# Kernel tuning notes

Hardware: AMD Instinct MI355X
Metric: run time of the kernel (lower is better)

## Reference

```python
import jax, jax.numpy as jnp
import numpy as np

B, Nv, Ne, Dv, De, Du = 8, 4096, 32768, 128, 128, 128
Dep, Dvp, Dup = 128, 128, 128


def setup_inputs() -> dict:
    key = jax.random.key(0)
    ks = jax.random.split(key, 11)
    s = 0.02
    return {
        "nodes": jax.random.normal(ks[0], (B, Nv, Dv), jnp.float32),
        "edges": jax.random.normal(ks[1], (B, Ne, De), jnp.float32),
        "global_u": jax.random.normal(ks[2], (B, Du), jnp.float32),
        "edge_rs": jax.random.randint(ks[3], (B, Ne, 2), 0, Nv, jnp.int32),
        "edge_masks": jax.random.randint(ks[4], (B, Ne, 1), 0, 2, jnp.int32),
        "W_edge": jax.random.normal(ks[5], (De + 2 * Dv + Du, Dep), jnp.float32) * s,
        "b_edge": jnp.zeros((Dep,), jnp.float32),
        "W_node": jax.random.normal(ks[6], (Dep + Dv + Du, Dvp), jnp.float32) * s,
        "b_node": jnp.zeros((Dvp,), jnp.float32),
        "W_glob": jax.random.normal(ks[7], (Dep + Dvp + Du, Dup), jnp.float32) * s,
        "b_glob": jnp.zeros((Dup,), jnp.float32),
    }


def reference(nodes, edges, global_u, edge_rs, edge_masks,
              W_edge, b_edge, W_node, b_node, W_glob, b_glob):
    recv = edge_rs[..., 0]  # (B,Ne)
    send = edge_rs[..., 1]
    # gather receiver / sender node features: (B,Ne,Dv)
    r_nodes = jnp.take_along_axis(nodes, jnp.broadcast_to(recv[..., None], (B, Ne, Dv)), axis=1)
    s_nodes = jnp.take_along_axis(nodes, jnp.broadcast_to(send[..., None], (B, Ne, Dv)), axis=1)
    u_e = jnp.broadcast_to(global_u[:, None, :], (B, Ne, Du))

    # edge block: MLP on concat -> (B,Ne,Dep)
    edge_in = jnp.concatenate([edges, r_nodes, s_nodes, u_e], -1)
    edges_p = jax.nn.relu(edge_in @ W_edge + b_edge)

    # e2v merge: masked segment-sum of edges onto receiver nodes -> (B,Nv,Dep)
    mask = edge_masks.astype(edges_p.dtype)  # (B,Ne,1)
    e2v = jax.vmap(lambda e, r: jax.ops.segment_sum(e, r, num_segments=Nv))(edges_p * mask, recv)

    # node block
    u_n = jnp.broadcast_to(global_u[:, None, :], (B, Nv, Du))
    node_in = jnp.concatenate([e2v, nodes, u_n], -1)
    nodes_p = jax.nn.relu(node_in @ W_node + b_node)

    # global block: sum-pool edges and nodes
    e2u = edges_p.sum(axis=1)  # (B,Dep)
    v2u = nodes_p.sum(axis=1)  # (B,Dvp)
    global_in = jnp.concatenate([e2u, v2u, global_u], -1)
    global_u_p = jax.nn.relu(global_in @ W_glob + b_glob)

    return (nodes_p, edges_p, global_u_p)
```

## Files before the change

kernel.cpp:

```cpp
#include <hip/hip_runtime.h>
#include <hip/hip_bf16.h>

#define B  8
#define NV 4096
#define NE 32768
#define D  128
#define KE2 384
#define KN2 256
#define KG 384

using short8 = __attribute__((ext_vector_type(8))) short;
using f32x4  = __attribute__((ext_vector_type(4))) float;

__device__ inline unsigned short f2bf(float f) {
    unsigned u = __builtin_bit_cast(unsigned, f);
    u += 0x7FFFu + ((u >> 16) & 1u);
    return (unsigned short)(u >> 16);
}

__device__ inline short8 cvt8(float4 a, float4 b) {
    union { __hip_bfloat162 h[4]; short8 v; } u;
    u.h[0] = __float22bfloat162_rn(make_float2(a.x, a.y));
    u.h[1] = __float22bfloat162_rn(make_float2(a.z, a.w));
    u.h[2] = __float22bfloat162_rn(make_float2(b.x, b.y));
    u.h[3] = __float22bfloat162_rn(make_float2(b.z, b.w));
    return u.v;
}

__global__ __launch_bounds__(256) void prep_weights(
    const float* __restrict__ We, const float* __restrict__ Wn,
    unsigned short* __restrict__ WtE, unsigned short* __restrict__ WtN)
{
    const int idx = blockIdx.x * 256 + threadIdx.x;
    {
        const int n = idx / KE2, k = idx % KE2;
        WtE[idx] = f2bf(We[(size_t)k * D + n]);
    }
    if (idx < 128 * KN2) {
        const int n = idx >> 8, k = idx & 255;
        WtN[idx] = f2bf(Wn[(size_t)k * D + n]);
    }
}

__global__ __launch_bounds__(128) void bias_kernel(
    const float* __restrict__ gu,
    const float* __restrict__ We, const float* __restrict__ be,
    const float* __restrict__ Wn, const float* __restrict__ bn,
    float* __restrict__ bias_e, float* __restrict__ bias_n)
{
    const int b = blockIdx.x, n = threadIdx.x;
    float se = be[n], sn = bn[n];
    for (int k = 0; k < D; ++k) {
        const float uk = gu[(size_t)b * D + k];
        se += uk * We[(size_t)(KE2 + k) * D + n];
        sn += uk * Wn[(size_t)(KN2 + k) * D + n];
    }
    bias_e[(size_t)b * D + n] = se;
    bias_n[(size_t)b * D + n] = sn;
}

__global__ __launch_bounds__(256) void hist_kernel(
    const int* __restrict__ edge_rs, const int* __restrict__ edge_masks,
    int* __restrict__ cnt)
{
    const int idx = blockIdx.x * 256 + threadIdx.x;
    if (edge_masks[idx]) {
        const int b = idx >> 15;
        const int r = edge_rs[2 * idx];
        atomicAdd(cnt + b * NV + r, 1);
    }
}

__global__ __launch_bounds__(1024) void scan_kernel(
    const int* __restrict__ cnt, int* __restrict__ off, int* __restrict__ cur)
{
    const int b = blockIdx.x, t = threadIdx.x;
    __shared__ int part[1024];
    int4 c = *(const int4*)(cnt + b * NV + t * 4);
    const int s0 = c.x, s1 = s0 + c.y, s2 = s1 + c.z, s3 = s2 + c.w;
    part[t] = s3;
    __syncthreads();
    #pragma unroll
    for (int d = 1; d < 1024; d <<= 1) {
        const int v = (t >= d) ? part[t - d] : 0;
        __syncthreads();
        part[t] += v;
        __syncthreads();
    }
    const int base = part[t] - s3;
    int* o = off + b * (NV + 1) + t * 4;
    o[0] = base; o[1] = base + s0; o[2] = base + s1; o[3] = base + s2;
    int4 cc = { base, base + s0, base + s1, base + s2 };
    *(int4*)(cur + b * NV + t * 4) = cc;
    if (t == 1023) off[b * (NV + 1) + NV] = part[1023];
}

__global__ __launch_bounds__(256) void scatter_kernel(
    const int* __restrict__ edge_rs, const int* __restrict__ edge_masks,
    int* __restrict__ cur, int* __restrict__ elist)
{
    const int idx = blockIdx.x * 256 + threadIdx.x;
    if (edge_masks[idx]) {
        const int b = idx >> 15;
        const int e = idx & (NE - 1);
        const int r = edge_rs[2 * idx];
        const int pos = atomicAdd(cur + b * NV + r, 1);
        elist[b * NE + pos] = e;
    }
}

__global__ __launch_bounds__(512, 4) void edge_kernel(
    const float* __restrict__ nodes,
    const float* __restrict__ edges,
    const int*   __restrict__ edge_rs,
    const unsigned short* __restrict__ WtE,
    const float* __restrict__ bias_e,
    float* __restrict__ edges_p,
    float* __restrict__ pe)
{
    __shared__ unsigned short Albuf[2][128 * 64];
    __shared__ unsigned short Wlbuf[2][128 * 64];

    const int tid = threadIdx.x;
    const int b   = blockIdx.y;
    const int e0  = blockIdx.x * 128;

    const int srow = tid >> 2;
    const int sq   = tid & 3;
    const int sX   = (srow & 7) << 3;

    const int2 rs = ((const int2*)edge_rs)[(size_t)b * NE + e0 + srow];
    const float* aseg0 = edges + ((size_t)b * NE + e0 + srow) * D;
    const float* aseg1 = nodes + ((size_t)b * NV + rs.x) * D;
    const float* aseg2 = nodes + ((size_t)b * NV + rs.y) * D;

    const int lane = tid & 63;
    const int wv   = tid >> 6;
    const int wr   = wv >> 2, wc = wv & 3;
    const int lc   = lane & 15, lg = lane >> 4;
    const int lX   = (lc & 7) << 3;

    float4 av[2];
    short8 wstg[2];

    auto loadA = [&](int t) {
        const float* seg = (t < 2) ? aseg0 : (t < 4) ? aseg1 : aseg2;
        const float* src = seg + (t & 1) * 64 + sq * 16;
        av[0] = *(const float4*)(src);
        av[1] = *(const float4*)(src + 4);
        av[0] = av[0];
    };
    auto loadA2 = [&](int t, float4& c0, float4& c1) {
        const float* seg = (t < 2) ? aseg0 : (t < 4) ? aseg1 : aseg2;
        const float* src = seg + (t & 1) * 64 + sq * 16;
        c0 = *(const float4*)(src + 8);
        c1 = *(const float4*)(src + 12);
    };
    auto loadW = [&](int t) {
        const unsigned short* src = WtE + (size_t)srow * KE2 + t * 64 + sq * 16;
        wstg[0] = *(const short8*)(src);
        wstg[1] = *(const short8*)(src + 8);
    };

    float4 av2[2];
    auto writeStage = [&](int buf) {
        unsigned short* Al = Albuf[buf];
        unsigned short* Wl = Wlbuf[buf];
        const int g0 = sq * 16;
        *(short8*)(Al + srow * 64 + ((g0    ) ^ sX)) = cvt8(av[0], av[1]);
        *(short8*)(Al + srow * 64 + ((g0 + 8) ^ sX)) = cvt8(av2[0], av2[1]);
        *(short8*)(Wl + srow * 64 + ((g0    ) ^ sX)) = wstg[0];
        *(short8*)(Wl + srow * 64 + ((g0 + 8) ^ sX)) = wstg[1];
    };

    f32x4 acc[4][2] = {};
    auto compute = [&](int buf) {
        const unsigned short* Al = Albuf[buf];
        const unsigned short* Wl = Wlbuf[buf];
        #pragma unroll
        for (int ksub = 0; ksub < 2; ++ksub) {
            const int k = ksub * 32 + lg * 8;
            short8 afr[4], bfr[2];
            #pragma unroll
            for (int mt = 0; mt < 4; ++mt)
                afr[mt] = *(const short8*)(Al + (wr * 64 + mt * 16 + lc) * 64 + (k ^ lX));
            #pragma unroll
            for (int nt = 0; nt < 2; ++nt)
                bfr[nt] = *(const short8*)(Wl + (wc * 32 + nt * 16 + lc) * 64 + (k ^ lX));
            #pragma unroll
            for (int mt = 0; mt < 4; ++mt)
                #pragma unroll
                for (int nt = 0; nt < 2; ++nt)
                    acc[mt][nt] = __builtin_amdgcn_mfma_f32_16x16x32_bf16(
                                      afr[mt], bfr[nt], acc[mt][nt], 0, 0, 0);
        }
    };

    loadA(0); loadA2(0, av2[0], av2[1]); loadW(0); writeStage(0);
    __syncthreads();
    #pragma unroll
    for (int t = 0; t < 6; ++t) {
        if (t < 5) { loadA(t + 1); loadA2(t + 1, av2[0], av2[1]); loadW(t + 1); }
        compute(t & 1);
        if (t < 5) writeStage((t + 1) & 1);
        __syncthreads();
    }

    #pragma unroll
    for (int nt = 0; nt < 2; ++nt) {
        const int col = wc * 32 + nt * 16 + lc;
        const float bias = bias_e[(size_t)b * D + col];
        float csum = 0.f;
        #pragma unroll
        for (int mt = 0; mt < 4; ++mt)
            #pragma unroll
            for (int r = 0; r < 4; ++r) {
                const int row = wr * 64 + mt * 16 + lg * 4 + r;
                const float v = fmaxf(acc[mt][nt][r] + bias, 0.f);
                edges_p[((size_t)b * NE + e0 + row) * D + col] = v;
                csum += v;
            }
        csum += __shfl_xor(csum, 16);
        csum += __shfl_xor(csum, 32);
        if (lg == 0)
            pe[(((size_t)b * 256 + blockIdx.x) * 2 + wr) * D + col] = csum;
    }
}

__global__ __launch_bounds__(512, 4) void node_kernel(
    const float* __restrict__ nodes,
    const float* __restrict__ edges_p,
    const int*   __restrict__ off,
    const int*   __restrict__ elist,
    const unsigned short* __restrict__ WtN,
    const float* __restrict__ bias_n,
    float* __restrict__ nodes_p,
    float* __restrict__ pn)
{
    __shared__ unsigned short Albuf[2][128 * 64];
    __shared__ unsigned short Wlbuf[2][128 * 64];

    const int tid = threadIdx.x;
    const int b   = blockIdx.y;
    const int n0  = blockIdx.x * 128;

    const int srow = tid >> 2;
    const int sq   = tid & 3;
    const int sX   = (srow & 7) << 3;

    const int vtx = n0 + srow;
    const int p0  = off[b * (NV + 1) + vtx];
    const int p1  = off[b * (NV + 1) + vtx + 1];
    const float* nsrc = nodes + ((size_t)b * NV + vtx) * D;

    const int lane = tid & 63;
    const int wv   = tid >> 6;
    const int wr   = wv >> 2, wc = wv & 3;
    const int lc   = lane & 15, lg = lane >> 4;
    const int lX   = (lc & 7) << 3;

    float4 av[2], av2[2];
    short8 wstg[2];

    auto loadA = [&](int t) {
        if (t < 2) {
            float4 s0 = {}, s1 = {}, s2 = {}, s3 = {};
            const int koff = (t & 1) * 64 + sq * 16;
            for (int p = p0; p < p1; ++p) {
                const int e = elist[b * NE + p];
                const float* src = edges_p + ((size_t)b * NE + e) * D + koff;
                const float4 x0 = *(const float4*)(src);
                const float4 x1 = *(const float4*)(src + 4);
                const float4 x2 = *(const float4*)(src + 8);
                const float4 x3 = *(const float4*)(src + 12);
                s0.x += x0.x; s0.y += x0.y; s0.z += x0.z; s0.w += x0.w;
                s1.x += x1.x; s1.y += x1.y; s1.z += x1.z; s1.w += x1.w;
                s2.x += x2.x; s2.y += x2.y; s2.z += x2.z; s2.w += x2.w;
                s3.x += x3.x; s3.y += x3.y; s3.z += x3.z; s3.w += x3.w;
            }
            av[0] = s0; av[1] = s1; av2[0] = s2; av2[1] = s3;
        } else {
            const float* src = nsrc + (t - 2) * 64 + sq * 16;
            av[0]  = *(const float4*)(src);
            av[1]  = *(const float4*)(src + 4);
            av2[0] = *(const float4*)(src + 8);
            av2[1] = *(const float4*)(src + 12);
        }
    };
    auto loadW = [&](int t) {
        const unsigned short* src = WtN + (size_t)srow * KN2 + t * 64 + sq * 16;
        wstg[0] = *(const short8*)(src);
        wstg[1] = *(const short8*)(src + 8);
    };
    auto writeStage = [&](int buf) {
        unsigned short* Al = Albuf[buf];
        unsigned short* Wl = Wlbuf[buf];
        const int g0 = sq * 16;
        *(short8*)(Al + srow * 64 + ((g0    ) ^ sX)) = cvt8(av[0], av[1]);
        *(short8*)(Al + srow * 64 + ((g0 + 8) ^ sX)) = cvt8(av2[0], av2[1]);
        *(short8*)(Wl + srow * 64 + ((g0    ) ^ sX)) = wstg[0];
        *(short8*)(Wl + srow * 64 + ((g0 + 8) ^ sX)) = wstg[1];
    };

    f32x4 acc[4][2] = {};
    auto compute = [&](int buf) {
        const unsigned short* Al = Albuf[buf];
        const unsigned short* Wl = Wlbuf[buf];
        #pragma unroll
        for (int ksub = 0; ksub < 2; ++ksub) {
            const int k = ksub * 32 + lg * 8;
            short8 afr[4], bfr[2];
            #pragma unroll
            for (int mt = 0; mt < 4; ++mt)
                afr[mt] = *(const short8*)(Al + (wr * 64 + mt * 16 + lc) * 64 + (k ^ lX));
            #pragma unroll
            for (int nt = 0; nt < 2; ++nt)
                bfr[nt] = *(const short8*)(Wl + (wc * 32 + nt * 16 + lc) * 64 + (k ^ lX));
            #pragma unroll
            for (int mt = 0; mt < 4; ++mt)
                #pragma unroll
                for (int nt = 0; nt < 2; ++nt)
                    acc[mt][nt] = __builtin_amdgcn_mfma_f32_16x16x32_bf16(
                                      afr[mt], bfr[nt], acc[mt][nt], 0, 0, 0);
        }
    };

    loadA(0); loadW(0); writeStage(0);
    __syncthreads();
    #pragma unroll
    for (int t = 0; t < 4; ++t) {
        if (t < 3) { loadA(t + 1); loadW(t + 1); }
        compute(t & 1);
        if (t < 3) writeStage((t + 1) & 1);
        __syncthreads();
    }

    #pragma unroll
    for (int nt = 0; nt < 2; ++nt) {
        const int col = wc * 32 + nt * 16 + lc;
        const float bias = bias_n[(size_t)b * D + col];
        float csum = 0.f;
        #pragma unroll
        for (int mt = 0; mt < 4; ++mt)
            #pragma unroll
            for (int r = 0; r < 4; ++r) {
                const int row = wr * 64 + mt * 16 + lg * 4 + r;
                const float v = fmaxf(acc[mt][nt][r] + bias, 0.f);
                nodes_p[((size_t)b * NV + n0 + row) * D + col] = v;
                csum += v;
            }
        csum += __shfl_xor(csum, 16);
        csum += __shfl_xor(csum, 32);
        if (lg == 0)
            pn[(((size_t)b * 32 + blockIdx.x) * 2 + wr) * D + col] = csum;
    }
}

__global__ __launch_bounds__(128) void reduce_kernel(
    const float* __restrict__ pe, const float* __restrict__ pn,
    float* __restrict__ e2u, float* __restrict__ v2u)
{
    const int b = blockIdx.x, j = threadIdx.x;
    float s = 0.f;
    for (int i = 0; i < 512; ++i) s += pe[((size_t)b * 512 + i) * D + j];
    e2u[(size_t)b * D + j] = s;
    float t = 0.f;
    for (int i = 0; i < 64; ++i) t += pn[((size_t)b * 64 + i) * D + j];
    v2u[(size_t)b * D + j] = t;
}

__global__ __launch_bounds__(128) void glob_kernel(
    const float* __restrict__ e2u,
    const float* __restrict__ v2u,
    const float* __restrict__ gu,
    const float* __restrict__ W_glob,
    const float* __restrict__ b_glob,
    float* __restrict__ glob_p)
{
    __shared__ float gin[KG];
    const int b = blockIdx.x;
    const int j = threadIdx.x;

    gin[j      ] = e2u[(size_t)b * D + j];
    gin[j + 128] = v2u[(size_t)b * D + j];
    gin[j + 256] = gu [(size_t)b * D + j];
    __syncthreads();

    float acc = b_glob[j];
    #pragma unroll 4
    for (int k = 0; k < KG; ++k)
        acc += gin[k] * W_glob[(size_t)k * D + j];
    glob_p[(size_t)b * D + j] = fmaxf(acc, 0.f);
}

extern "C" void kernel_launch(void* const* d_in, const int* in_sizes, int n_in,
                              void* d_out, int out_size, void* d_ws, size_t ws_size,
                              hipStream_t stream) {
    const float* nodes      = (const float*)d_in[0];
    const float* edges      = (const float*)d_in[1];
    const float* gu         = (const float*)d_in[2];
    const int*   edge_rs    = (const int*)d_in[3];
    const int*   edge_masks = (const int*)d_in[4];
    const float* W_edge     = (const float*)d_in[5];
    const float* b_edge     = (const float*)d_in[6];
    const float* W_node     = (const float*)d_in[7];
    const float* b_node     = (const float*)d_in[8];
    const float* W_glob     = (const float*)d_in[9];
    const float* b_glob     = (const float*)d_in[10];

    float* out     = (float*)d_out;
    float* nodes_p = out;
    float* edges_p = out + (size_t)B * NV * D;
    float* glob_p  = edges_p + (size_t)B * NE * D;

    int*   cnt    = (int*)d_ws;
    int*   off    = cnt + (size_t)B * NV;
    int*   cur    = off + (size_t)B * (NV + 1);
    int*   elist  = cur + (size_t)B * NV;
    float* e2u    = (float*)(elist + (size_t)B * NE);
    float* v2u    = e2u + (size_t)B * D;
    float* bias_e = v2u + (size_t)B * D;
    float* bias_n = bias_e + (size_t)B * D;
    float* pe     = bias_n + (size_t)B * D;
    float* pn     = pe + (size_t)B * 512 * D;
    unsigned short* WtE = (unsigned short*)(pn + (size_t)B * 64 * D);
    unsigned short* WtN = WtE + 128 * KE2;

    hipMemsetAsync(cnt, 0, (size_t)B * NV * sizeof(int), stream);

    prep_weights<<<(128 * KE2) / 256, 256, 0, stream>>>(W_edge, W_node, WtE, WtN);
    bias_kernel<<<B, 128, 0, stream>>>(gu, W_edge, b_edge, W_node, b_node, bias_e, bias_n);
    hist_kernel<<<(B * NE) / 256, 256, 0, stream>>>(edge_rs, edge_masks, cnt);
    scan_kernel<<<B, 1024, 0, stream>>>(cnt, off, cur);
    scatter_kernel<<<(B * NE) / 256, 256, 0, stream>>>(edge_rs, edge_masks, cur, elist);

    dim3 eg(NE / 128, B);
    edge_kernel<<<eg, 512, 0, stream>>>(nodes, edges, edge_rs,
                                        WtE, bias_e, edges_p, pe);
    dim3 ng(NV / 128, B);
    node_kernel<<<ng, 512, 0, stream>>>(nodes, edges_p, off, elist,
                                        WtN, bias_n, nodes_p, pn);
    reduce_kernel<<<B, 128, 0, stream>>>(pe, pn, e2u, v2u);
    glob_kernel<<<B, 128, 0, stream>>>(e2u, v2u, gu, W_glob, b_glob, glob_p);
}
```

Baseline: 199.4 us.

## Load weight fragments directly from global memory, dropping LDS weight staging

Both the edge and node GEMM kernels stop staging the bf16 weight tiles through shared memory. Each wave now reads its B fragments straight from global memory, which the cache should serve since the weights are small and shared by all blocks. This halves LDS use per block, and the launch bounds are raised to allow more resident blocks per CU. The trade-off is global-load latency inside the MFMA loop that is no longer hidden by the double buffer, plus possibly more register pressure under the tighter occupancy bound.

```diff
diff --git a/kernel.cpp b/kernel.cpp
--- a/kernel.cpp
+++ b/kernel.cpp
@@ -109,7 +109,7 @@
     }
 }
 
-__global__ __launch_bounds__(512, 4) void edge_kernel(
+__global__ __launch_bounds__(512, 8) void edge_kernel(
     const float* __restrict__ nodes,
     const float* __restrict__ edges,
     const int*   __restrict__ edge_rs,
@@ -119,7 +119,6 @@
     float* __restrict__ pe)
 {
     __shared__ unsigned short Albuf[2][128 * 64];
-    __shared__ unsigned short Wlbuf[2][128 * 64];
 
     const int tid = threadIdx.x;
     const int b   = blockIdx.y;
@@ -140,53 +139,37 @@
     const int lc   = lane & 15, lg = lane >> 4;
     const int lX   = (lc & 7) << 3;
 
-    float4 av[2];
-    short8 wstg[2];
+    float4 av[2], av2[2];
 
     auto loadA = [&](int t) {
         const float* seg = (t < 2) ? aseg0 : (t < 4) ? aseg1 : aseg2;
         const float* src = seg + (t & 1) * 64 + sq * 16;
-        av[0] = *(const float4*)(src);
-        av[1] = *(const float4*)(src + 4);
-        av[0] = av[0];
-    };
-    auto loadA2 = [&](int t, float4& c0, float4& c1) {
-        const float* seg = (t < 2) ? aseg0 : (t < 4) ? aseg1 : aseg2;
-        const float* src = seg + (t & 1) * 64 + sq * 16;
-        c0 = *(const float4*)(src + 8);
-        c1 = *(const float4*)(src + 12);
-    };
-    auto loadW = [&](int t) {
-        const unsigned short* src = WtE + (size_t)srow * KE2 + t * 64 + sq * 16;
-        wstg[0] = *(const short8*)(src);
-        wstg[1] = *(const short8*)(src + 8);
-    };
-
-    float4 av2[2];
+        av[0]  = *(const float4*)(src);
+        av[1]  = *(const float4*)(src + 4);
+        av2[0] = *(const float4*)(src + 8);
+        av2[1] = *(const float4*)(src + 12);
+    };
     auto writeStage = [&](int buf) {
         unsigned short* Al = Albuf[buf];
-        unsigned short* Wl = Wlbuf[buf];
         const int g0 = sq * 16;
         *(short8*)(Al + srow * 64 + ((g0    ) ^ sX)) = cvt8(av[0], av[1]);
         *(short8*)(Al + srow * 64 + ((g0 + 8) ^ sX)) = cvt8(av2[0], av2[1]);
-        *(short8*)(Wl + srow * 64 + ((g0    ) ^ sX)) = wstg[0];
-        *(short8*)(Wl + srow * 64 + ((g0 + 8) ^ sX)) = wstg[1];
     };
 
     f32x4 acc[4][2] = {};
-    auto compute = [&](int buf) {
+    auto compute = [&](int buf, int t) {
         const unsigned short* Al = Albuf[buf];
-        const unsigned short* Wl = Wlbuf[buf];
         #pragma unroll
         for (int ksub = 0; ksub < 2; ++ksub) {
             const int k = ksub * 32 + lg * 8;
             short8 afr[4], bfr[2];
             #pragma unroll
+            for (int nt = 0; nt < 2; ++nt)
+                bfr[nt] = *(const short8*)(WtE + (size_t)(wc * 32 + nt * 16 + lc) * KE2
+                                               + t * 64 + k);
+            #pragma unroll
             for (int mt = 0; mt < 4; ++mt)
                 afr[mt] = *(const short8*)(Al + (wr * 64 + mt * 16 + lc) * 64 + (k ^ lX));
-            #pragma unroll
-            for (int nt = 0; nt < 2; ++nt)
-                bfr[nt] = *(const short8*)(Wl + (wc * 32 + nt * 16 + lc) * 64 + (k ^ lX));
             #pragma unroll
             for (int mt = 0; mt < 4; ++mt)
                 #pragma unroll
@@ -196,12 +179,12 @@
         }
     };
 
-    loadA(0); loadA2(0, av2[0], av2[1]); loadW(0); writeStage(0);
+    loadA(0); writeStage(0);
     __syncthreads();
     #pragma unroll
     for (int t = 0; t < 6; ++t) {
-        if (t < 5) { loadA(t + 1); loadA2(t + 1, av2[0], av2[1]); loadW(t + 1); }
-        compute(t & 1);
+        if (t < 5) loadA(t + 1);
+        compute(t & 1, t);
         if (t < 5) writeStage((t + 1) & 1);
         __syncthreads();
     }
@@ -227,7 +210,7 @@
     }
 }
 
-__global__ __launch_bounds__(512, 4) void node_kernel(
+__global__ __launch_bounds__(512, 6) void node_kernel(
     const float* __restrict__ nodes,
     const float* __restrict__ edges_p,
     const int*   __restrict__ off,
@@ -238,7 +221,6 @@
     float* __restrict__ pn)
 {
     __shared__ unsigned short Albuf[2][128 * 64];
-    __shared__ unsigned short Wlbuf[2][128 * 64];
 
     const int tid = threadIdx.x;
     const int b   = blockIdx.y;
@@ -260,7 +242,6 @@
     const int lX   = (lc & 7) << 3;
 
     float4 av[2], av2[2];
-    short8 wstg[2];
 
     auto loadA = [&](int t) {
         if (t < 2) {
@@ -287,35 +268,27 @@
             av2[1] = *(const float4*)(src + 12);
         }
     };
-    auto loadW = [&](int t) {
-        const unsigned short* src = WtN + (size_t)srow * KN2 + t * 64 + sq * 16;
-        wstg[0] = *(const short8*)(src);
-        wstg[1] = *(const short8*)(src + 8);
-    };
     auto writeStage = [&](int buf) {
         unsigned short* Al = Albuf[buf];
-        unsigned short* Wl = Wlbuf[buf];
         const int g0 = sq * 16;
         *(short8*)(Al + srow * 64 + ((g0    ) ^ sX)) = cvt8(av[0], av[1]);
         *(short8*)(Al + srow * 64 + ((g0 + 8) ^ sX)) = cvt8(av2[0], av2[1]);
-        *(short8*)(Wl + srow * 64 + ((g0    ) ^ sX)) = wstg[0];
-        *(short8*)(Wl + srow * 64 + ((g0 + 8) ^ sX)) = wstg[1];
     };
 
     f32x4 acc[4][2] = {};
-    auto compute = [&](int buf) {
+    auto compute = [&](int buf, int t) {
         const unsigned short* Al = Albuf[buf];
-        const unsigned short* Wl = Wlbuf[buf];
         #pragma unroll
         for (int ksub = 0; ksub < 2; ++ksub) {
             const int k = ksub * 32 + lg * 8;
             short8 afr[4], bfr[2];
             #pragma unroll
+            for (int nt = 0; nt < 2; ++nt)
+                bfr[nt] = *(const short8*)(WtN + (size_t)(wc * 32 + nt * 16 + lc) * KN2
+                                               + t * 64 + k);
+            #pragma unroll
             for (int mt = 0; mt < 4; ++mt)
                 afr[mt] = *(const short8*)(Al + (wr * 64 + mt * 16 + lc) * 64 + (k ^ lX));
-            #pragma unroll
-            for (int nt = 0; nt < 2; ++nt)
-                bfr[nt] = *(const short8*)(Wl + (wc * 32 + nt * 16 + lc) * 64 + (k ^ lX));
             #pragma unroll
             for (int mt = 0; mt < 4; ++mt)
                 #pragma unroll
@@ -325,12 +298,12 @@
         }
     };
 
-    loadA(0); loadW(0); writeStage(0);
+    loadA(0); writeStage(0);
     __syncthreads();
     #pragma unroll
     for (int t = 0; t < 4; ++t) {
-        if (t < 3) { loadA(t + 1); loadW(t + 1); }
-        compute(t & 1);
+        if (t < 3) loadA(t + 1);
+        compute(t & 1, t);
         if (t < 3) writeStage((t + 1) & 1);
         __syncthreads();
     }
```

After: 301.3 us. 1.51x slower.

## Shrink edge kernel LDS, retile node kernel to 64 rows, split reduce

Applied to the files above, without the earlier changes.

The edge kernel drops the double-buffered weight tile for a single buffer and adds an extra barrier before each stage write. This cuts LDS use and raises the occupancy hint from 4 to 6 blocks per CU. The node kernel moves to 64-vertex tiles with 256 threads, so the grid has twice as many blocks to spread the irregular segment-sum gather across CUs, and the reduce kernel now uses two halves plus a shared-memory combine. The trade-off is an extra sync per stage in the edge kernel, which serializes the stage write against compute, and more register pressure from the tighter launch bound.

```diff
diff --git a/kernel.cpp b/kernel.cpp
--- a/kernel.cpp
+++ b/kernel.cpp
@@ -109,7 +109,7 @@
     }
 }
 
-__global__ __launch_bounds__(512, 4) void edge_kernel(
+__global__ __launch_bounds__(512, 6) void edge_kernel(
     const float* __restrict__ nodes,
     const float* __restrict__ edges,
     const int*   __restrict__ edge_rs,
@@ -119,7 +119,7 @@
     float* __restrict__ pe)
 {
     __shared__ unsigned short Albuf[2][128 * 64];
-    __shared__ unsigned short Wlbuf[2][128 * 64];
+    __shared__ unsigned short Wlbuf[128 * 64];
 
     const int tid = threadIdx.x;
     const int b   = blockIdx.y;
@@ -140,53 +140,47 @@
     const int lc   = lane & 15, lg = lane >> 4;
     const int lX   = (lc & 7) << 3;
 
-    float4 av[2];
+    float4 av[2], av2[2];
     short8 wstg[2];
 
     auto loadA = [&](int t) {
         const float* seg = (t < 2) ? aseg0 : (t < 4) ? aseg1 : aseg2;
         const float* src = seg + (t & 1) * 64 + sq * 16;
-        av[0] = *(const float4*)(src);
-        av[1] = *(const float4*)(src + 4);
-        av[0] = av[0];
-    };
-    auto loadA2 = [&](int t, float4& c0, float4& c1) {
-        const float* seg = (t < 2) ? aseg0 : (t < 4) ? aseg1 : aseg2;
-        const float* src = seg + (t & 1) * 64 + sq * 16;
-        c0 = *(const float4*)(src + 8);
-        c1 = *(const float4*)(src + 12);
+        av[0]  = *(const float4*)(src);
+        av[1]  = *(const float4*)(src + 4);
+        av2[0] = *(const float4*)(src + 8);
+        av2[1] = *(const float4*)(src + 12);
     };
     auto loadW = [&](int t) {
         const unsigned short* src = WtE + (size_t)srow * KE2 + t * 64 + sq * 16;
         wstg[0] = *(const short8*)(src);
         wstg[1] = *(const short8*)(src + 8);
     };
-
-    float4 av2[2];
-    auto writeStage = [&](int buf) {
+    auto writeStageA = [&](int buf) {
         unsigned short* Al = Albuf[buf];
-        unsigned short* Wl = Wlbuf[buf];
         const int g0 = sq * 16;
         *(short8*)(Al + srow * 64 + ((g0    ) ^ sX)) = cvt8(av[0], av[1]);
         *(short8*)(Al + srow * 64 + ((g0 + 8) ^ sX)) = cvt8(av2[0], av2[1]);
-        *(short8*)(Wl + srow * 64 + ((g0    ) ^ sX)) = wstg[0];
-        *(short8*)(Wl + srow * 64 + ((g0 + 8) ^ sX)) = wstg[1];
+    };
+    auto writeStageW = [&]() {
+        const int g0 = sq * 16;
+        *(short8*)(Wlbuf + srow * 64 + ((g0    ) ^ sX)) = wstg[0];
+        *(short8*)(Wlbuf + srow * 64 + ((g0 + 8) ^ sX)) = wstg[1];
     };
 
     f32x4 acc[4][2] = {};
     auto compute = [&](int buf) {
         const unsigned short* Al = Albuf[buf];
-        const unsigned short* Wl = Wlbuf[buf];
         #pragma unroll
         for (int ksub = 0; ksub < 2; ++ksub) {
             const int k = ksub * 32 + lg * 8;
             short8 afr[4], bfr[2];
             #pragma unroll
+            for (int nt = 0; nt < 2; ++nt)
+                bfr[nt] = *(const short8*)(Wlbuf + (wc * 32 + nt * 16 + lc) * 64 + (k ^ lX));
+            #pragma unroll
             for (int mt = 0; mt < 4; ++mt)
                 afr[mt] = *(const short8*)(Al + (wr * 64 + mt * 16 + lc) * 64 + (k ^ lX));
-            #pragma unroll
-            for (int nt = 0; nt < 2; ++nt)
-                bfr[nt] = *(const short8*)(Wl + (wc * 32 + nt * 16 + lc) * 64 + (k ^ lX));
             #pragma unroll
             for (int mt = 0; mt < 4; ++mt)
                 #pragma unroll
@@ -196,14 +190,18 @@
         }
     };
 
-    loadA(0); loadA2(0, av2[0], av2[1]); loadW(0); writeStage(0);
+    loadA(0); loadW(0); writeStageA(0); writeStageW();
     __syncthreads();
     #pragma unroll
     for (int t = 0; t < 6; ++t) {
-        if (t < 5) { loadA(t + 1); loadA2(t + 1, av2[0], av2[1]); loadW(t + 1); }
+        if (t < 5) { loadA(t + 1); loadW(t + 1); }
         compute(t & 1);
-        if (t < 5) writeStage((t + 1) & 1);
-        __syncthreads();
+        if (t < 5) {
+            __syncthreads();
+            writeStageA((t + 1) & 1);
+            writeStageW();
+            __syncthreads();
+        }
     }
 
     #pragma unroll
@@ -227,7 +225,7 @@
     }
 }
 
-__global__ __launch_bounds__(512, 4) void node_kernel(
+__global__ __launch_bounds__(256, 3) void node_kernel(
     const float* __restrict__ nodes,
     const float* __restrict__ edges_p,
     const int*   __restrict__ off,
@@ -237,35 +235,38 @@
     float* __restrict__ nodes_p,
     float* __restrict__ pn)
 {
-    __shared__ unsigned short Albuf[2][128 * 64];
+    __shared__ unsigned short Albuf[2][64 * 64];
     __shared__ unsigned short Wlbuf[2][128 * 64];
 
     const int tid = threadIdx.x;
     const int b   = blockIdx.y;
-    const int n0  = blockIdx.x * 128;
-
-    const int srow = tid >> 2;
-    const int sq   = tid & 3;
-    const int sX   = (srow & 7) << 3;
-
-    const int vtx = n0 + srow;
+    const int n0  = blockIdx.x * 64;
+
+    const int srowA = tid >> 2;
+    const int sqA   = tid & 3;
+    const int sXA   = (srowA & 7) << 3;
+    const int srowW = tid >> 1;
+    const int sqW   = tid & 1;
+    const int sXW   = (srowW & 7) << 3;
+
+    const int vtx = n0 + srowA;
     const int p0  = off[b * (NV + 1) + vtx];
     const int p1  = off[b * (NV + 1) + vtx + 1];
     const float* nsrc = nodes + ((size_t)b * NV + vtx) * D;
 
     const int lane = tid & 63;
     const int wv   = tid >> 6;
-    const int wr   = wv >> 2, wc = wv & 3;
+    const int wr   = wv >> 1, wc = wv & 1;
     const int lc   = lane & 15, lg = lane >> 4;
     const int lX   = (lc & 7) << 3;
 
     float4 av[2], av2[2];
-    short8 wstg[2];
+    short8 wstg[4];
 
     auto loadA = [&](int t) {
         if (t < 2) {
             float4 s0 = {}, s1 = {}, s2 = {}, s3 = {};
-            const int koff = (t & 1) * 64 + sq * 16;
+            const int koff = (t & 1) * 64 + sqA * 16;
             for (int p = p0; p < p1; ++p) {
                 const int e = elist[b * NE + p];
                 const float* src = edges_p + ((size_t)b * NE + e) * D + koff;
@@ -280,7 +281,7 @@
             }
             av[0] = s0; av[1] = s1; av2[0] = s2; av2[1] = s3;
         } else {
-            const float* src = nsrc + (t - 2) * 64 + sq * 16;
+            const float* src = nsrc + (t - 2) * 64 + sqA * 16;
             av[0]  = *(const float4*)(src);
             av[1]  = *(const float4*)(src + 4);
             av2[0] = *(const float4*)(src + 8);
@@ -288,38 +289,43 @@
         }
     };
     auto loadW = [&](int t) {
-        const unsigned short* src = WtN + (size_t)srow * KN2 + t * 64 + sq * 16;
+        const unsigned short* src = WtN + (size_t)srowW * KN2 + t * 64 + sqW * 32;
         wstg[0] = *(const short8*)(src);
         wstg[1] = *(const short8*)(src + 8);
+        wstg[2] = *(const short8*)(src + 16);
+        wstg[3] = *(const short8*)(src + 24);
     };
     auto writeStage = [&](int buf) {
         unsigned short* Al = Albuf[buf];
+        const int gA = sqA * 16;
+        *(short8*)(Al + srowA * 64 + ((gA    ) ^ sXA)) = cvt8(av[0], av[1]);
+        *(short8*)(Al + srowA * 64 + ((gA + 8) ^ sXA)) = cvt8(av2[0], av2[1]);
         unsigned short* Wl = Wlbuf[buf];
-        const int g0 = sq * 16;
-        *(short8*)(Al + srow * 64 + ((g0    ) ^ sX)) = cvt8(av[0], av[1]);
-        *(short8*)(Al + srow * 64 + ((g0 + 8) ^ sX)) = cvt8(av2[0], av2[1]);
-        *(short8*)(Wl + srow * 64 + ((g0    ) ^ sX)) = wstg[0];
-        *(short8*)(Wl + srow * 64 + ((g0 + 8) ^ sX)) = wstg[1];
-    };
-
-    f32x4 acc[4][2] = {};
+        const int gW = sqW * 32;
+        *(short8*)(Wl + srowW * 64 + ((gW     ) ^ sXW)) = wstg[0];
+        *(short8*)(Wl + srowW * 64 + ((gW + 8 ) ^ sXW)) = wstg[1];
+        *(short8*)(Wl + srowW * 64 + ((gW + 16) ^ sXW)) = wstg[2];
+        *(short8*)(Wl + srowW * 64 + ((gW + 24) ^ sXW)) = wstg[3];
+    };
+
+    f32x4 acc[2][4] = {};
     auto compute = [&](int buf) {
         const unsigned short* Al = Albuf[buf];
         const unsigned short* Wl = Wlbuf[buf];
         #pragma unroll
         for (int ksub = 0; ksub < 2; ++ksub) {
             const int k = ksub * 32 + lg * 8;
-            short8 afr[4], bfr[2];
-            #pragma unroll
-            for (int mt = 0; mt < 4; ++mt)
-                afr[mt] = *(const short8*)(Al + (wr * 64 + mt * 16 + lc) * 64 + (k ^ lX));
-            #pragma unroll
-            for (int nt = 0; nt < 2; ++nt)
-                bfr[nt] = *(const short8*)(Wl + (wc * 32 + nt * 16 + lc) * 64 + (k ^ lX));
-            #pragma unroll
-            for (int mt = 0; mt < 4; ++mt)
+            short8 afr[2], bfr[4];
+            #pragma unroll
+            for (int mt = 0; mt < 2; ++mt)
+                afr[mt] = *(const short8*)(Al + (wr * 32 + mt * 16 + lc) * 64 + (k ^ lX));
+            #pragma unroll
+            for (int nt = 0; nt < 4; ++nt)
+                bfr[nt] = *(const short8*)(Wl + (wc * 64 + nt * 16 + lc) * 64 + (k ^ lX));
+            #pragma unroll
+            for (int mt = 0; mt < 2; ++mt)
                 #pragma unroll
-                for (int nt = 0; nt < 2; ++nt)
+                for (int nt = 0; nt < 4; ++nt)
                     acc[mt][nt] = __builtin_amdgcn_mfma_f32_16x16x32_bf16(
                                       afr[mt], bfr[nt], acc[mt][nt], 0, 0, 0);
         }
@@ -331,20 +337,22 @@
     for (int t = 0; t < 4; ++t) {
         if (t < 3) { loadA(t + 1); loadW(t + 1); }
         compute(t & 1);
-        if (t < 3) writeStage((t + 1) & 1);
-        __syncthreads();
+        if (t < 3) {
+            writeStage((t + 1) & 1);
+            __syncthreads();
+        }
     }
 
     #pragma unroll
-    for (int nt = 0; nt < 2; ++nt) {
-        const int col = wc * 32 + nt * 16 + lc;
+    for (int nt = 0; nt < 4; ++nt) {
+        const int col = wc * 64 + nt * 16 + lc;
         const float bias = bias_n[(size_t)b * D + col];
         float csum = 0.f;
         #pragma unroll
-        for (int mt = 0; mt < 4; ++mt)
+        for (int mt = 0; mt < 2; ++mt)
             #pragma unroll
             for (int r = 0; r < 4; ++r) {
-                const int row = wr * 64 + mt * 16 + lg * 4 + r;
+                const int row = wr * 32 + mt * 16 + lg * 4 + r;
                 const float v = fmaxf(acc[mt][nt][r] + bias, 0.f);
                 nodes_p[((size_t)b * NV + n0 + row) * D + col] = v;
                 csum += v;
@@ -352,21 +360,31 @@
         csum += __shfl_xor(csum, 16);
         csum += __shfl_xor(csum, 32);
         if (lg == 0)
-            pn[(((size_t)b * 32 + blockIdx.x) * 2 + wr) * D + col] = csum;
-    }
-}
-
-__global__ __launch_bounds__(128) void reduce_kernel(
+            pn[(((size_t)b * 64 + blockIdx.x) * 2 + wr) * D + col] = csum;
+    }
+}
+
+__global__ __launch_bounds__(256) void reduce_kernel(
     const float* __restrict__ pe, const float* __restrict__ pn,
     float* __restrict__ e2u, float* __restrict__ v2u)
 {
-    const int b = blockIdx.x, j = threadIdx.x;
+    __shared__ float redE[2][128], redN[2][128];
+    const int b = blockIdx.x;
+    const int j = threadIdx.x & 127;
+    const int h = threadIdx.x >> 7;
     float s = 0.f;
-    for (int i = 0; i < 512; ++i) s += pe[((size_t)b * 512 + i) * D + j];
-    e2u[(size_t)b * D + j] = s;
+    for (int i = h * 256; i < h * 256 + 256; ++i)
+        s += pe[((size_t)b * 512 + i) * D + j];
     float t = 0.f;
-    for (int i = 0; i < 64; ++i) t += pn[((size_t)b * 64 + i) * D + j];
-    v2u[(size_t)b * D + j] = t;
+    for (int i = h * 64; i < h * 64 + 64; ++i)
+        t += pn[((size_t)b * 128 + i) * D + j];
+    redE[h][j] = s;
+    redN[h][j] = t;
+    __syncthreads();
+    if (h == 0) {
+        e2u[(size_t)b * D + j] = redE[0][j] + redE[1][j];
+        v2u[(size_t)b * D + j] = redN[0][j] + redN[1][j];
+    }
 }
 
 __global__ __launch_bounds__(128) void glob_kernel(
@@ -423,7 +441,7 @@
     float* bias_n = bias_e + (size_t)B * D;
     float* pe     = bias_n + (size_t)B * D;
     float* pn     = pe + (size_t)B * 512 * D;
-    unsigned short* WtE = (unsigned short*)(pn + (size_t)B * 64 * D);
+    unsigned short* WtE = (unsigned short*)(pn + (size_t)B * 128 * D);
     unsigned short* WtN = WtE + 128 * KE2;
 
     hipMemsetAsync(cnt, 0, (size_t)B * NV * sizeof(int), stream);
@@ -437,9 +455,9 @@
     dim3 eg(NE / 128, B);
     edge_kernel<<<eg, 512, 0, stream>>>(nodes, edges, edge_rs,
                                         WtE, bias_e, edges_p, pe);
-    dim3 ng(NV / 128, B);
-    node_kernel<<<ng, 512, 0, stream>>>(nodes, edges_p, off, elist,
+    dim3 ng(NV / 64, B);
+    node_kernel<<<ng, 256, 0, stream>>>(nodes, edges_p, off, elist,
                                         WtN, bias_n, nodes_p, pn);
-    reduce_kernel<<<B, 128, 0, stream>>>(pe, pn, e2u, v2u);
+    reduce_kernel<<<B, 256, 0, stream>>>(pe, pn, e2u, v2u);
     glob_kernel<<<B, 128, 0, stream>>>(e2u, v2u, gu, W_glob, b_glob, glob_p);
 }
```

After: 221.8 us. 1.11x slower.
